# Kernel tuning notes

Hardware: AMD Instinct MI355X
Metric: run time of the kernel (lower is better)

## Reference

```python
import jax, jax.numpy as jnp
import numpy as np

H = 256  # hidden_size
IN = 256  # input_size
OUT = 128  # output_size


def _gru_cell(x, h, Wx, bx, Wh, bh):
    # x: (B, in), h: (B, H); Wx: (3H, in), Wh: (3H, H)
    xt = x @ Wx.T + bx  # (B, 3H)
    ht = h @ Wh.T + bh  # (B, 3H)
    xr, xz, xn = jnp.split(xt, 3, axis=1)
    hr, hz, hn = jnp.split(ht, 3, axis=1)
    r = jax.nn.sigmoid(xr + hr)
    z = jax.nn.sigmoid(xz + hz)
    n = jnp.tanh(xn + r * hn)
    return z * h + (1.0 - z) * n


def setup_inputs() -> dict:
    key = jax.random.key(0)
    ks = jax.random.split(key, 12)
    std = 1.0 / np.sqrt(H)
    u = lambda k, shape: jax.random.uniform(k, shape, jnp.float32, -std, std)
    return {
        "x": jax.random.normal(ks[0], (128, 1024, IN), jnp.float32),
        "Wx0": u(ks[1], (3 * H, IN)), "bx0": u(ks[2], (3 * H,)),
        "Wh0": u(ks[3], (3 * H, H)), "bh0": u(ks[4], (3 * H,)),
        "Wx1": u(ks[5], (3 * H, H)), "bx1": u(ks[6], (3 * H,)),
        "Wh1": u(ks[7], (3 * H, H)), "bh1": u(ks[8], (3 * H,)),
        "Wo": u(ks[9], (OUT, H)), "bo": u(ks[10], (OUT,)),
    }


def reference(x, Wx0, bx0, Wh0, bh0, Wx1, bx1, Wh1, bh1, Wo, bo):
    B = x.shape[0]
    h_init = (jnp.zeros((B, H), x.dtype), jnp.zeros((B, H), x.dtype))

    def step(carry, x_t):
        h0, h1 = carry
        h0 = _gru_cell(x_t, h0, Wx0, bx0, Wh0, bh0)
        h1 = _gru_cell(h0, h1, Wx1, bx1, Wh1, bh1)
        return (h0, h1), None

    # scan over time: x transposed to (T, B, in)
    (h0, h1), _ = jax.lax.scan(step, h_init, jnp.swapaxes(x, 0, 1))
    return h1 @ Wo.T + bo
```

## Files before the change

### kernel.cpp

```cpp
#include <hip/hip_runtime.h>
#include <stdint.h>


#define NPAIR 64
#define WSLOT 4

#define XR0_OFF 0
#define XR1_OFF 393216
#define HR0_OFF 786432
#define CTR_OFF 851968
#define FLG_OFF 856064

#if defined(__has_builtin)
#if __has_builtin(__builtin_amdgcn_fdot2)
#define USE_DOT2 1
#endif
#endif

typedef uint32_t u32x16 __attribute__((ext_vector_type(16)));
typedef _Float16 h2_t __attribute__((ext_vector_type(2)));
union H2U { uint32_t u; h2_t h; };
union FU  { uint32_t u; float f; };

__device__ __forceinline__ float bf2f(uint16_t b){ FU v; v.u=(uint32_t)b<<16; return v.f; }
__device__ __forceinline__ uint16_t f2bf(float f){
    FU v; v.f=f; uint32_t r=v.u+0x7fffu+((v.u>>16)&1u); return (uint16_t)(r>>16);
}
__device__ __forceinline__ float sigmoid_f(float x){ return 1.0f/(1.0f+__expf(-x)); }
__device__ __forceinline__ float tanh_f(float x){
    float ax=fabsf(x); float e=__expf(-2.0f*ax);
    float t=(1.0f-e)/(1.0f+e); return x<0.0f?-t:t;
}
__device__ __forceinline__ float dot2acc(uint32_t w, uint32_t v, float acc){
#ifdef USE_DOT2
    H2U a,b; a.u=w; b.u=v;
    return __builtin_amdgcn_fdot2(a.h, b.h, acc, false);
#else
    FU x0,x1,y0,y1;
    x0.u=w<<16; x1.u=w&0xffff0000u; y0.u=v<<16; y1.u=v&0xffff0000u;
    acc=fmaf(x0.f,y0.f,acc); return fmaf(x1.f,y1.f,acc);
#endif
}
__device__ __forceinline__ uint32_t cvt_bfpair(uint32_t raw){
#ifdef USE_DOT2
    FU lo,hi; lo.u=raw<<16; hi.u=raw&0xffff0000u;
    H2U r; r.h[0]=(_Float16)lo.f; r.h[1]=(_Float16)hi.f; return r.u;
#else
    return raw;
#endif
}
__device__ __forceinline__ uint32_t packpair(float lo, float hi){
#ifdef USE_DOT2
    H2U r; r.h[0]=(_Float16)lo; r.h[1]=(_Float16)hi; return r.u;
#else
    return (uint32_t)f2bf(lo) | ((uint32_t)f2bf(hi)<<16);
#endif
}
__device__ __forceinline__ u32x16 load16_bf(const uint4* p){
    uint4 a=p[0], b=p[1], c=p[2], d=p[3];
    u32x16 v;
    v[0]=cvt_bfpair(a.x);  v[1]=cvt_bfpair(a.y);  v[2]=cvt_bfpair(a.z);  v[3]=cvt_bfpair(a.w);
    v[4]=cvt_bfpair(b.x);  v[5]=cvt_bfpair(b.y);  v[6]=cvt_bfpair(b.z);  v[7]=cvt_bfpair(b.w);
    v[8]=cvt_bfpair(c.x);  v[9]=cvt_bfpair(c.y);  v[10]=cvt_bfpair(c.z); v[11]=cvt_bfpair(c.w);
    v[12]=cvt_bfpair(d.x); v[13]=cvt_bfpair(d.y); v[14]=cvt_bfpair(d.z); v[15]=cvt_bfpair(d.w);
    return v;
}
__device__ __forceinline__ u32x16 load16_f32(const float2* p){
    u32x16 v;
#define LF(i) v[i] = packpair(p[i].x, p[i].y)
    LF(0);LF(1);LF(2);LF(3);LF(4);LF(5);LF(6);LF(7);
    LF(8);LF(9);LF(10);LF(11);LF(12);LF(13);LF(14);LF(15);
#undef LF
    return v;
}

#define RLX_LD(p)    __hip_atomic_load((p),        __ATOMIC_RELAXED, __HIP_MEMORY_SCOPE_AGENT)
#define RLX_ST(p,v)  __hip_atomic_store((p), (v),  __ATOMIC_RELAXED, __HIP_MEMORY_SCOPE_AGENT)

#define DOT16(WR, WZ, WN, G)                                                      \
    _Pragma("unroll")                                                             \
    for (int q = 0; q < 4; ++q) {                                                 \
        uint4 va = pa[4*(G)+q], vb = pb[4*(G)+q];                                 \
        ar0 = dot2acc(WR[4*q+0], va.x, ar0); ar1 = dot2acc(WR[4*q+0], vb.x, ar1); \
        az0 = dot2acc(WZ[4*q+0], va.x, az0); az1 = dot2acc(WZ[4*q+0], vb.x, az1); \
        an0 = dot2acc(WN[4*q+0], va.x, an0); an1 = dot2acc(WN[4*q+0], vb.x, an1); \
        ar0 = dot2acc(WR[4*q+1], va.y, ar0); ar1 = dot2acc(WR[4*q+1], vb.y, ar1); \
        az0 = dot2acc(WZ[4*q+1], va.y, az0); az1 = dot2acc(WZ[4*q+1], vb.y, az1); \
        an0 = dot2acc(WN[4*q+1], va.y, an0); an1 = dot2acc(WN[4*q+1], vb.y, an1); \
        ar0 = dot2acc(WR[4*q+2], va.z, ar0); ar1 = dot2acc(WR[4*q+2], vb.z, ar1); \
        az0 = dot2acc(WZ[4*q+2], va.z, az0); az1 = dot2acc(WZ[4*q+2], vb.z, az1); \
        an0 = dot2acc(WN[4*q+2], va.z, an0); an1 = dot2acc(WN[4*q+2], vb.z, an1); \
        ar0 = dot2acc(WR[4*q+3], va.w, ar0); ar1 = dot2acc(WR[4*q+3], vb.w, ar1); \
        az0 = dot2acc(WZ[4*q+3], va.w, az0); az1 = dot2acc(WZ[4*q+3], vb.w, az1); \
        an0 = dot2acc(WN[4*q+3], va.w, an0); an1 = dot2acc(WN[4*q+3], vb.w, an1); \
    }

__global__ void probe_init(const uint32_t* __restrict__ w,
                           uint32_t* __restrict__ ctr,
                           uint32_t* __restrict__ flag) {
    int i = threadIdx.x;
    for (int k = i; k < 4096; k += 1024) ctr[k] = 0u;
    if (i == 0) {
        int c = 0;
        for (int j = 0; j < 64; ++j) {
            uint32_t e = (w[j] >> 7) & 0xFFu;
            c += (e >= 0x60u && e <= 0x7Cu) ? 1 : 0;
        }
        flag[0] = (c >= 32) ? 1u : 0u;
    }
}

__global__ void __launch_bounds__(512, 2)
gru6(const void* __restrict__ xin,
     const void* __restrict__ Wx0, const void* __restrict__ bx0,
     const void* __restrict__ Wh0, const void* __restrict__ bh0,
     const void* __restrict__ Wx1, const void* __restrict__ bx1,
     const void* __restrict__ Wh1, const void* __restrict__ bh1,
     const void* __restrict__ Wo,  const void* __restrict__ bo,
     void* __restrict__ out,
     uint32_t* __restrict__ ws)
{
    const int tid  = threadIdx.x;
    const int pair = blockIdx.x & (NPAIR - 1);
    const int role = blockIdx.x >> 6;
    const int p    = tid >> 1;
    const int hs   = tid & 1;

    float*    XRING0 = (float*)(ws + XR0_OFF) + pair * 6144;
    float*    XRING1 = (float*)(ws + XR1_OFF) + pair * 6144;
    uint32_t* HRING  = ws + HR0_OFF + pair * 1024;
    uint32_t* CTR    = ws + CTR_OFF;
    const int isbf   = (int)ws[FLG_OFF];

    uint32_t* myctr   = CTR + role * 1024 + pair * 16;
    uint32_t* prodctr = CTR + (role - 1) * 1024 + pair * 16;
    uint32_t* consctr = CTR + (role + 1) * 1024 + pair * 16;

    const void* Wsel; const void* bsel;
    if      (role == 0) { Wsel = Wx0; bsel = bx0; }
    else if (role == 1) { Wsel = Wh0; bsel = bh0; }
    else if (role == 2) { Wsel = Wx1; bsel = bx1; }
    else                { Wsel = Wh1; bsel = bh1; }

    u32x16 wr0,wr1,wr2,wr3, wz0,wz1,wz2,wz3, wn0,wn1,wn2,wn3;
    float br, bz, bn;
    if (isbf) {
        const uint4* W4 = (const uint4*)Wsel;
        const uint4* r0 = W4 + (size_t)p * 32 + hs * 16;
        const uint4* r1 = W4 + (size_t)(p + 256) * 32 + hs * 16;
        const uint4* r2 = W4 + (size_t)(p + 512) * 32 + hs * 16;
        wr0=load16_bf(r0);    wr1=load16_bf(r0+4);  wr2=load16_bf(r0+8);  wr3=load16_bf(r0+12);
        wz0=load16_bf(r1);    wz1=load16_bf(r1+4);  wz2=load16_bf(r1+8);  wz3=load16_bf(r1+12);
        wn0=load16_bf(r2);    wn1=load16_bf(r2+4);  wn2=load16_bf(r2+8);  wn3=load16_bf(r2+12);
        const uint16_t* bs = (const uint16_t*)bsel;
        br = bf2f(bs[p]); bz = bf2f(bs[p+256]); bn = bf2f(bs[p+512]);
    } else {
        const float2* W2 = (const float2*)Wsel;
        const float2* r0 = W2 + (size_t)p * 128 + hs * 64;
        const float2* r1 = W2 + (size_t)(p + 256) * 128 + hs * 64;
        const float2* r2 = W2 + (size_t)(p + 512) * 128 + hs * 64;
        wr0=load16_f32(r0);    wr1=load16_f32(r0+16); wr2=load16_f32(r0+32); wr3=load16_f32(r0+48);
        wz0=load16_f32(r1);    wz1=load16_f32(r1+16); wz2=load16_f32(r1+32); wz3=load16_f32(r1+48);
        wn0=load16_f32(r2);    wn1=load16_f32(r2+16); wn2=load16_f32(r2+32); wn3=load16_f32(r2+48);
        const float* bs = (const float*)bsel;
        br = bs[p]; bz = bs[p+256]; bn = bs[p+512];
    }

    __shared__ __align__(16) uint32_t sb[544];

    if (role == 0 || role == 2) {
        const uint32_t* xs32 = (const uint32_t*)xin;
        const float2*   xsf  = (const float2*)xin;
        const int bglob = pair * 2 + (tid >> 7);
        const int i128  = tid & 127;
        const int spos  = (tid >> 7) * 136 + i128 + ((i128 >> 6) << 2);
        uint32_t xpref = 0, nxt = 0; bool have = false;
        if (role == 0 && tid < 256) {
            if (isbf) xpref = cvt_bfpair(xs32[(size_t)bglob * 131072 + i128]);
            else { float2 f = xsf[(size_t)bglob * 131072 + i128]; xpref = packpair(f.x, f.y); }
        }
        float* outring = (role == 0) ? XRING0 : XRING1;
        uint32_t prog_seen = 0;

        for (int t = 0; t < 1024; ++t) {
            if (t >= WSLOT && prog_seen + (WSLOT - 1) < (uint32_t)t) {
                do { prog_seen = RLX_LD(consctr);
                     if (prog_seen + (WSLOT - 1) < (uint32_t)t) __builtin_amdgcn_s_sleep(2);
                } while (prog_seen + (WSLOT - 1) < (uint32_t)t);
            }
            if (tid < 256) {
                uint32_t pk;
                if (role == 0) pk = xpref;
                else {
                    if (have) pk = nxt;
                    else {
                        uint32_t c;
                        do { c = RLX_LD(prodctr);
                             if (c < (uint32_t)(t + 1)) __builtin_amdgcn_s_sleep(2);
                        } while (c < (uint32_t)(t + 1));
                        pk = RLX_LD(HRING + (t & 3) * 256 + tid);
                    }
                }
                sb[(t & 1) * 272 + spos] = pk;
            }
            asm volatile("s_waitcnt vmcnt(0)" ::: "memory");
            __syncthreads();
            if (tid == 0) RLX_ST(myctr, (uint32_t)t);
            if (tid < 256 && t < 1023) {
                if (role == 0) {
                    if (isbf) xpref = cvt_bfpair(xs32[(size_t)bglob * 131072 + (t+1)*128 + i128]);
                    else { float2 f = xsf[(size_t)bglob * 131072 + (t+1)*128 + i128]; xpref = packpair(f.x, f.y); }
                } else {
                    uint32_t c = RLX_LD(prodctr);
                    have = (c >= (uint32_t)(t + 2));
                    if (have) nxt = RLX_LD(HRING + ((t+1) & 3) * 256 + tid);
                }
            }
            float ar0=0,ar1=0,az0=0,az1=0,an0=0,an1=0;
            {
                const uint4* pa = ((const uint4*)&sb[(t & 1) * 272]) + hs * 17;
                const uint4* pb = pa + 34;
                DOT16(wr0,wz0,wn0,0); DOT16(wr1,wz1,wn1,1);
                DOT16(wr2,wz2,wn2,2); DOT16(wr3,wz3,wn3,3);
            }
            float R0 = ar0 + __shfl_xor(ar0,1), R1 = ar1 + __shfl_xor(ar1,1);
            float Z0 = az0 + __shfl_xor(az0,1), Z1 = az1 + __shfl_xor(az1,1);
            float N0 = an0 + __shfl_xor(an0,1), N1 = an1 + __shfl_xor(an1,1);
            float sr = (hs ? R1 : R0) + br;
            float sz = (hs ? Z1 : Z0) + bz;
            float sn = (hs ? N1 : N0) + bn;
            float* d = outring + (t & 3) * 1536;
            RLX_ST(d + 2*p + hs,        sr);
            RLX_ST(d + 512 + 2*p + hs,  sz);
            RLX_ST(d + 1024 + 2*p + hs, sn);
        }
        asm volatile("s_waitcnt vmcnt(0)" ::: "memory");
        __syncthreads();
        if (tid == 0) RLX_ST(myctr, 1024u);
    } else {
        const float* xrng = (role == 1) ? XRING0 : XRING1;
        float h_reg = 0.0f;
        for (int i = tid; i < 544; i += 512) sb[i] = 0u;
        bool have = false; float nr=0, nz=0, nn=0;
        uint32_t prog_seen = 0;
        const int hj   = p >> 1;
        const int hpos = hs * 136 + hj + ((hj >> 6) << 2);

        for (int t = 0; t < 1024; ++t) {
            if (role == 1 && t >= WSLOT && prog_seen + (WSLOT - 1) < (uint32_t)t) {
                do { prog_seen = RLX_LD(consctr);
                     if (prog_seen + (WSLOT - 1) < (uint32_t)t) __builtin_amdgcn_s_sleep(2);
                } while (prog_seen + (WSLOT - 1) < (uint32_t)t);
            }
            float xr, xz, xn;
            if (have) { xr = nr; xz = nz; xn = nn; }
            else {
                uint32_t c;
                do { c = RLX_LD(prodctr);
                     if (c < (uint32_t)(t + 1)) __builtin_amdgcn_s_sleep(2);
                } while (c < (uint32_t)(t + 1));
                const float* s = xrng + (t & 3) * 1536;
                xr = RLX_LD(s + 2*p + hs);
                xz = RLX_LD(s + 512 + 2*p + hs);
                xn = RLX_LD(s + 1024 + 2*p + hs);
            }
            asm volatile("s_waitcnt vmcnt(0)" ::: "memory");
            __syncthreads();
            if (tid == 0) RLX_ST(myctr, (uint32_t)t);
            if (t < 1023) {
                uint32_t c = RLX_LD(prodctr);
                have = (c >= (uint32_t)(t + 2));
                if (have) {
                    const float* s = xrng + ((t + 1) & 3) * 1536;
                    nr = RLX_LD(s + 2*p + hs);
                    nz = RLX_LD(s + 512 + 2*p + hs);
                    nn = RLX_LD(s + 1024 + 2*p + hs);
                }
            } else have = false;
            float ar0=0,ar1=0,az0=0,az1=0,an0=0,an1=0;
            {
                const uint4* pa = ((const uint4*)&sb[(t & 1) * 272]) + hs * 17;
                const uint4* pb = pa + 34;
                DOT16(wr0,wz0,wn0,0); DOT16(wr1,wz1,wn1,1);
                DOT16(wr2,wz2,wn2,2); DOT16(wr3,wz3,wn3,3);
            }
            float R0 = ar0 + __shfl_xor(ar0,1), R1 = ar1 + __shfl_xor(ar1,1);
            float Z0 = az0 + __shfl_xor(az0,1), Z1 = az1 + __shfl_xor(az1,1);
            float N0 = an0 + __shfl_xor(an0,1), N1 = an1 + __shfl_xor(an1,1);
            float r = sigmoid_f(xr + (hs ? R1 : R0) + br);
            float z = sigmoid_f(xz + (hs ? Z1 : Z0) + bz);
            float n = tanh_f(xn + r * ((hs ? N1 : N0) + bn));
            h_reg = z * h_reg + (1.0f - z) * n;
            float hp = __shfl_xor(h_reg, 2);
            if (!(tid & 2)) {
                uint32_t pk = packpair(h_reg, hp);
                sb[((t + 1) & 1) * 272 + hpos] = pk;
                if (role == 1)
                    RLX_ST(HRING + (t & 3) * 256 + hs * 128 + hj, pk);
            }
        }
        asm volatile("s_waitcnt vmcnt(0)" ::: "memory");
        __syncthreads();
        if (tid == 0) RLX_ST(myctr, 1024u);

        if (role == 3 && tid < 256) {
            const int j = tid >> 1, bb = tid & 1;
            const uint32_t* hv = &sb[bb * 136];
            float acc;
            if (isbf) {
                acc = bf2f(((const uint16_t*)bo)[j]);
                const uint32_t* wo = (const uint32_t*)Wo + j * 128;
#pragma unroll 8
                for (int c = 0; c < 128; ++c)
                    acc = dot2acc(cvt_bfpair(wo[c]), hv[c + ((c >> 6) << 2)], acc);
                ((uint16_t*)out)[(pair * 2 + bb) * 128 + j] = f2bf(acc);
            } else {
                acc = ((const float*)bo)[j];
                const float2* wo = (const float2*)Wo + j * 128;
#pragma unroll 8
                for (int c = 0; c < 128; ++c) {
                    float2 f = wo[c];
                    acc = dot2acc(packpair(f.x, f.y), hv[c + ((c >> 6) << 2)], acc);
                }
                ((float*)out)[(pair * 2 + bb) * 128 + j] = acc;
            }
        }
    }
}

extern "C" void kernel_launch(void* const* d_in, const int* in_sizes, int n_in,
                              void* d_out, int out_size, void* d_ws, size_t ws_size,
                              hipStream_t stream) {
    uint32_t* ws  = (uint32_t*)d_ws;
    uint32_t* CTR = ws + CTR_OFF;
    uint32_t* FLG = ws + FLG_OFF;

    probe_init<<<dim3(1), dim3(1024), 0, stream>>>((const uint32_t*)d_in[1], CTR, FLG);
    gru6<<<dim3(256), dim3(512), 0, stream>>>(
        d_in[0], d_in[1], d_in[2], d_in[3], d_in[4],
        d_in[5], d_in[6], d_in[7], d_in[8], d_in[9], d_in[10],
        d_out, ws);
}
```

Measured before the change: 3.033 ms.

## Replace producer counters with sequence-tagged 64-bit ring entries and fp16 payloads

```diff
diff --git a/kernel.cpp b/kernel.cpp
--- a/kernel.cpp
+++ b/kernel.cpp
@@ -3,13 +3,12 @@
 
 
 #define NPAIR 64
-#define WSLOT 4
 
 #define XR0_OFF 0
-#define XR1_OFF 393216
-#define HR0_OFF 786432
-#define CTR_OFF 851968
-#define FLG_OFF 856064
+#define XR1_OFF 262144
+#define HR0_OFF 524288
+#define CTR_OFF 655360
+#define FLG_OFF 659456
 
 #if defined(__has_builtin)
 #if __has_builtin(__builtin_amdgcn_fdot2)
@@ -76,6 +75,12 @@
 
 #define RLX_LD(p)    __hip_atomic_load((p),        __ATOMIC_RELAXED, __HIP_MEMORY_SCOPE_AGENT)
 #define RLX_ST(p,v)  __hip_atomic_store((p), (v),  __ATOMIC_RELAXED, __HIP_MEMORY_SCOPE_AGENT)
+__device__ __forceinline__ uint64_t RLX_LD64(const uint64_t* p){
+    return __hip_atomic_load(p, __ATOMIC_RELAXED, __HIP_MEMORY_SCOPE_AGENT);
+}
+__device__ __forceinline__ void RLX_ST64(uint64_t* p, uint64_t v){
+    __hip_atomic_store(p, v, __ATOMIC_RELAXED, __HIP_MEMORY_SCOPE_AGENT);
+}
 
 #define DOT16(WR, WZ, WN, G)                                                      \
     _Pragma("unroll")                                                             \
@@ -110,8 +115,8 @@
     }
 }
 
-__global__ void __launch_bounds__(512, 2)
-gru6(const void* __restrict__ xin,
+__global__ void __launch_bounds__(512) __attribute__((amdgpu_waves_per_eu(2, 2)))
+gru7(const void* __restrict__ xin,
      const void* __restrict__ Wx0, const void* __restrict__ bx0,
      const void* __restrict__ Wh0, const void* __restrict__ bh0,
      const void* __restrict__ Wx1, const void* __restrict__ bx1,
@@ -126,15 +131,14 @@
     const int p    = tid >> 1;
     const int hs   = tid & 1;
 
-    float*    XRING0 = (float*)(ws + XR0_OFF) + pair * 6144;
-    float*    XRING1 = (float*)(ws + XR1_OFF) + pair * 6144;
-    uint32_t* HRING  = ws + HR0_OFF + pair * 1024;
-    uint32_t* CTR    = ws + CTR_OFF;
-    const int isbf   = (int)ws[FLG_OFF];
-
-    uint32_t* myctr   = CTR + role * 1024 + pair * 16;
-    uint32_t* prodctr = CTR + (role - 1) * 1024 + pair * 16;
-    uint32_t* consctr = CTR + (role + 1) * 1024 + pair * 16;
+    uint64_t* XR0p = (uint64_t*)(ws + XR0_OFF) + pair * 2048;
+    uint64_t* XR1p = (uint64_t*)(ws + XR1_OFF) + pair * 2048;
+    uint64_t* HRp  = (uint64_t*)(ws + HR0_OFF) + pair * 1024;
+    uint32_t* CTR  = ws + CTR_OFF;
+    const int isbf = (int)ws[FLG_OFF];
+
+    uint32_t* myprg   = CTR + role * 1024 + pair * 16;
+    uint32_t* consprg = CTR + (role + 1) * 1024 + pair * 16;
 
     const void* Wsel; const void* bsel;
     if      (role == 0) { Wsel = Wx0; bsel = bx0; }
@@ -174,46 +178,48 @@
         const int bglob = pair * 2 + (tid >> 7);
         const int i128  = tid & 127;
         const int spos  = (tid >> 7) * 136 + i128 + ((i128 >> 6) << 2);
-        uint32_t xpref = 0, nxt = 0; bool have = false;
+        uint32_t xpref = 0;
+        uint2 pfh; pfh.x = 0; pfh.y = 0;
         if (role == 0 && tid < 256) {
             if (isbf) xpref = cvt_bfpair(xs32[(size_t)bglob * 131072 + i128]);
             else { float2 f = xsf[(size_t)bglob * 131072 + i128]; xpref = packpair(f.x, f.y); }
         }
-        float* outring = (role == 0) ? XRING0 : XRING1;
+        uint64_t* outring = (role == 0) ? XR0p : XR1p;
         uint32_t prog_seen = 0;
 
         for (int t = 0; t < 1024; ++t) {
-            if (t >= WSLOT && prog_seen + (WSLOT - 1) < (uint32_t)t) {
-                do { prog_seen = RLX_LD(consctr);
-                     if (prog_seen + (WSLOT - 1) < (uint32_t)t) __builtin_amdgcn_s_sleep(2);
-                } while (prog_seen + (WSLOT - 1) < (uint32_t)t);
+            if (t >= 4 && prog_seen + 3 < (uint32_t)t) {
+                do { prog_seen = RLX_LD(consprg);
+                     if (prog_seen + 3 < (uint32_t)t) __builtin_amdgcn_s_sleep(2);
+                } while (prog_seen + 3 < (uint32_t)t);
             }
             if (tid < 256) {
                 uint32_t pk;
                 if (role == 0) pk = xpref;
                 else {
-                    if (have) pk = nxt;
-                    else {
-                        uint32_t c;
-                        do { c = RLX_LD(prodctr);
-                             if (c < (uint32_t)(t + 1)) __builtin_amdgcn_s_sleep(2);
-                        } while (c < (uint32_t)(t + 1));
-                        pk = RLX_LD(HRING + (t & 3) * 256 + tid);
+                    uint2 v = pfh;
+                    const uint32_t want = (uint32_t)(t + 1);
+                    if (v.y != want) {
+                        const uint64_t* a = HRp + (t & 3) * 256 + tid;
+                        uint64_t u;
+                        do { u = RLX_LD64(a);
+                             v.x = (uint32_t)u; v.y = (uint32_t)(u >> 32);
+                             if (v.y != want) __builtin_amdgcn_s_sleep(1);
+                        } while (v.y != want);
                     }
+                    pk = v.x;
                 }
                 sb[(t & 1) * 272 + spos] = pk;
             }
-            asm volatile("s_waitcnt vmcnt(0)" ::: "memory");
             __syncthreads();
-            if (tid == 0) RLX_ST(myctr, (uint32_t)t);
+            if (tid == 0 && !(t & 1)) RLX_ST(myprg, (uint32_t)t);
             if (tid < 256 && t < 1023) {
                 if (role == 0) {
                     if (isbf) xpref = cvt_bfpair(xs32[(size_t)bglob * 131072 + (t+1)*128 + i128]);
                     else { float2 f = xsf[(size_t)bglob * 131072 + (t+1)*128 + i128]; xpref = packpair(f.x, f.y); }
                 } else {
-                    uint32_t c = RLX_LD(prodctr);
-                    have = (c >= (uint32_t)(t + 2));
-                    if (have) nxt = RLX_LD(HRING + ((t+1) & 3) * 256 + tid);
+                    uint64_t u = RLX_LD64(HRp + ((t + 1) & 3) * 256 + tid);
+                    pfh.x = (uint32_t)u; pfh.y = (uint32_t)(u >> 32);
                 }
             }
             float ar0=0,ar1=0,az0=0,az1=0,an0=0,an1=0;
@@ -229,54 +235,46 @@
             float sr = (hs ? R1 : R0) + br;
             float sz = (hs ? Z1 : Z0) + bz;
             float sn = (hs ? N1 : N0) + bn;
-            float* d = outring + (t & 3) * 1536;
-            RLX_ST(d + 2*p + hs,        sr);
-            RLX_ST(d + 512 + 2*p + hs,  sz);
-            RLX_ST(d + 1024 + 2*p + hs, sn);
-        }
-        asm volatile("s_waitcnt vmcnt(0)" ::: "memory");
-        __syncthreads();
-        if (tid == 0) RLX_ST(myctr, 1024u);
+            H2U lo; lo.h[0] = (_Float16)sr; lo.h[1] = (_Float16)sz;
+            H2U sn16; sn16.u = 0; sn16.h[0] = (_Float16)sn;
+            uint32_t hi = (sn16.u & 0xFFFFu) | (((uint32_t)(t + 1)) << 16);
+            RLX_ST64(outring + (t & 3) * 512 + 2 * p + hs,
+                     (uint64_t)lo.u | ((uint64_t)hi << 32));
+        }
     } else {
-        const float* xrng = (role == 1) ? XRING0 : XRING1;
+        const uint64_t* xr64 = (role == 1) ? XR0p : XR1p;
         float h_reg = 0.0f;
         for (int i = tid; i < 544; i += 512) sb[i] = 0u;
-        bool have = false; float nr=0, nz=0, nn=0;
+        uint2 pfx; pfx.x = 0; pfx.y = 0;
         uint32_t prog_seen = 0;
         const int hj   = p >> 1;
         const int hpos = hs * 136 + hj + ((hj >> 6) << 2);
 
         for (int t = 0; t < 1024; ++t) {
-            if (role == 1 && t >= WSLOT && prog_seen + (WSLOT - 1) < (uint32_t)t) {
-                do { prog_seen = RLX_LD(consctr);
-                     if (prog_seen + (WSLOT - 1) < (uint32_t)t) __builtin_amdgcn_s_sleep(2);
-                } while (prog_seen + (WSLOT - 1) < (uint32_t)t);
-            }
-            float xr, xz, xn;
-            if (have) { xr = nr; xz = nz; xn = nn; }
-            else {
-                uint32_t c;
-                do { c = RLX_LD(prodctr);
-                     if (c < (uint32_t)(t + 1)) __builtin_amdgcn_s_sleep(2);
-                } while (c < (uint32_t)(t + 1));
-                const float* s = xrng + (t & 3) * 1536;
-                xr = RLX_LD(s + 2*p + hs);
-                xz = RLX_LD(s + 512 + 2*p + hs);
-                xn = RLX_LD(s + 1024 + 2*p + hs);
-            }
-            asm volatile("s_waitcnt vmcnt(0)" ::: "memory");
+            if (role == 1 && t >= 4 && prog_seen + 3 < (uint32_t)t) {
+                do { prog_seen = RLX_LD(consprg);
+                     if (prog_seen + 3 < (uint32_t)t) __builtin_amdgcn_s_sleep(2);
+                } while (prog_seen + 3 < (uint32_t)t);
+            }
+            uint2 v = pfx;
+            const uint32_t want = (uint32_t)(t + 1);
+            if ((v.y >> 16) != want) {
+                const uint64_t* a = xr64 + (t & 3) * 512 + 2 * p + hs;
+                uint64_t u;
+                do { u = RLX_LD64(a);
+                     v.x = (uint32_t)u; v.y = (uint32_t)(u >> 32);
+                     if ((v.y >> 16) != want) __builtin_amdgcn_s_sleep(1);
+                } while ((v.y >> 16) != want);
+            }
+            H2U ua; ua.u = v.x;
+            H2U ub; ub.u = v.y & 0xFFFFu;
+            float xr = (float)ua.h[0], xz = (float)ua.h[1], xn = (float)ub.h[0];
             __syncthreads();
-            if (tid == 0) RLX_ST(myctr, (uint32_t)t);
+            if (tid == 0 && !(t & 1)) RLX_ST(myprg, (uint32_t)t);
             if (t < 1023) {
-                uint32_t c = RLX_LD(prodctr);
-                have = (c >= (uint32_t)(t + 2));
-                if (have) {
-                    const float* s = xrng + ((t + 1) & 3) * 1536;
-                    nr = RLX_LD(s + 2*p + hs);
-                    nz = RLX_LD(s + 512 + 2*p + hs);
-                    nn = RLX_LD(s + 1024 + 2*p + hs);
-                }
-            } else have = false;
+                uint64_t u = RLX_LD64(xr64 + ((t + 1) & 3) * 512 + 2 * p + hs);
+                pfx.x = (uint32_t)u; pfx.y = (uint32_t)(u >> 32);
+            }
             float ar0=0,ar1=0,az0=0,az1=0,an0=0,an1=0;
             {
                 const uint4* pa = ((const uint4*)&sb[(t & 1) * 272]) + hs * 17;
@@ -296,12 +294,12 @@
                 uint32_t pk = packpair(h_reg, hp);
                 sb[((t + 1) & 1) * 272 + hpos] = pk;
                 if (role == 1)
-                    RLX_ST(HRING + (t & 3) * 256 + hs * 128 + hj, pk);
-            }
-        }
-        asm volatile("s_waitcnt vmcnt(0)" ::: "memory");
+                    RLX_ST64(HRp + (t & 3) * 256 + hs * 128 + hj,
+                             (uint64_t)pk | ((uint64_t)(t + 1) << 32));
+            }
+        }
         __syncthreads();
-        if (tid == 0) RLX_ST(myctr, 1024u);
+        if (tid == 0) RLX_ST(myprg, 1024u);
 
         if (role == 3 && tid < 256) {
             const int j = tid >> 1, bb = tid & 1;
@@ -336,7 +334,7 @@
     uint32_t* FLG = ws + FLG_OFF;
 
     probe_init<<<dim3(1), dim3(1024), 0, stream>>>((const uint32_t*)d_in[1], CTR, FLG);
-    gru6<<<dim3(256), dim3(512), 0, stream>>>(
+    gru7<<<dim3(256), dim3(512), 0, stream>>>(
         d_in[0], d_in[1], d_in[2], d_in[3], d_in[4],
         d_in[5], d_in[6], d_in[7], d_in[8], d_in[9], d_in[10],
         d_out, ws);
```

Measured after the change: 2.711 ms. 1.12x faster.
